# Kernel optimization log

Hardware: AMD Instinct MI355X
Metric: run time of the kernel (lower is better)

The kernel has to match this reference:

```python
import jax, jax.numpy as jnp
import numpy as np

B, D, H, C, P, HP = 65536, 256, 512, 10, 10, 128


def setup_inputs() -> dict:
    key = jax.random.key(0)
    ks = jax.random.split(key, 6)
    return {
        "x": jax.random.normal(ks[0], (B, D), jnp.float32),
        "Wt1": jax.random.normal(ks[1], (D, H), jnp.float32) * (1.0 / np.sqrt(D)),
        "bt1": jnp.zeros((H,), jnp.float32),
        "Wt2": jax.random.normal(ks[2], (H, C), jnp.float32) * (1.0 / np.sqrt(H)),
        "bt2": jnp.zeros((C,), jnp.float32),
        "Wp1": jax.random.normal(ks[3], (P, D, HP), jnp.float32) * (1.0 / np.sqrt(D)),
        "bp1": jnp.zeros((P, HP), jnp.float32),
        "Wp2": jax.random.normal(ks[4], (P, HP, C), jnp.float32) * (1.0 / np.sqrt(HP)),
        "bp2": jnp.zeros((P, C), jnp.float32),
        "repair_direction_dict": jax.random.randint(ks[5], (P, 2), 0, C, jnp.int32),
    }


def _get_bitmap(out, rdd):
    # torch.topk(out, 2): indices of the two largest logits per row
    _, idx = jax.lax.top_k(out, 2)                                  # [B, 2]
    # is_in[b, p] = all(idx[b] == rdd[p])  (exact top-2 pair match)
    is_in = jnp.all(idx[:, None, :] == rdd[None, :, :], axis=-1)     # [B, P]
    no_match = ~jnp.any(is_in, axis=-1)                              # [B]
    # fallback for unmatched rows: top-1 index equals rdd[:, 0]
    fallback = idx[:, :1] == rdd[None, :, 0]                         # [B, P]
    return jnp.where(no_match[:, None], fallback, is_in)             # bool [B, P]


def reference(x, Wt1, bt1, Wt2, bt2, Wp1, bp1, Wp2, bp2, repair_direction_dict):
    # target net forward: out = target_net(x)
    out = jnp.maximum(x @ Wt1 + bt1, 0.0) @ Wt2 + bt2                # [B, C]
    # bitmap computed under no_grad in the original -> stop_gradient
    bitmap = jax.lax.stop_gradient(
        _get_bitmap(out, repair_direction_dict)
    ).astype(out.dtype)                                              # [B, P]
    # each patch net runs on the FULL batch (as in the original), then the
    # bitmap gates the scatter-add combine: out[bits] += p_out[bits]
    h = jnp.maximum(jnp.einsum('bd,pdh->pbh', x, Wp1) + bp1[:, None, :], 0.0)  # [P, B, HP]
    p_out = jnp.einsum('pbh,phc->pbc', h, Wp2) + bp2[:, None, :]     # [P, B, C]
    return out + jnp.einsum('bp,pbc->bc', bitmap, p_out)             # [B, C]
```

## Files before the change

kernel.cpp:

```cpp
#include <hip/hip_runtime.h>

typedef unsigned int u32;
typedef unsigned short u16;
typedef _Float16 f16;
typedef __attribute__((ext_vector_type(8))) _Float16 f16x8;
typedef __attribute__((ext_vector_type(4))) float f32x4;

#define MARGIN 1e-2f
#define LSC 2048.0f
#define LSCI (1.0f/2048.0f)

__device__ __forceinline__ u16 f16b(float f) {
    return __builtin_bit_cast(u16, (f16)f);
}
__device__ __forceinline__ f32x4 MF(f16x8 a, f16x8 b, f32x4 c) {
    return __builtin_amdgcn_mfma_f32_16x16x32_f16(a, b, c, 0, 0, 0);
}
__device__ __forceinline__ uint4 pack8(const u16 v[8]) {
    uint4 pk;
    pk.x = (u32)v[0] | ((u32)v[1] << 16);
    pk.y = (u32)v[2] | ((u32)v[3] << 16);
    pk.z = (u32)v[4] | ((u32)v[5] << 16);
    pk.w = (u32)v[6] | ((u32)v[7] << 16);
    return pk;
}

__global__ __launch_bounds__(256) void conv_kernel(
    const float* __restrict__ Wt1, const float* __restrict__ Wp1,
    const float* __restrict__ Wt2, const float* __restrict__ Wp2,
    u16* __restrict__ wt1f, u16* __restrict__ wt1g, u16* __restrict__ wp1f,
    u16* __restrict__ wt2f, u16* __restrict__ wt2g, u16* __restrict__ wp2f,
    u32* __restrict__ gcnt)
{
    __shared__ float tile[64][68];
    const int t = threadIdx.x;
    const int b = blockIdx.x;

    if (b == 112) {
        if (t == 0) gcnt[0] = 0;
        for (int cc = t; cc < 1024; cc += 256) {
            int kk = cc >> 6, l = cc & 63, ln = l & 15, quad = l >> 4;
            u16 vh[8], vl[8];
            #pragma unroll
            for (int j = 0; j < 8; ++j) {
                int k = kk * 32 + quad * 8 + j;
                float f = (ln < 10) ? Wt2[k * 10 + ln] : 0.f;
                f16 h = (f16)f;
                vh[j] = __builtin_bit_cast(u16, h);
                vl[j] = f16b(LSC * (f - (float)h));
            }
            *(uint4*)(wt2f + kk * 512 + l * 8) = pack8(vh);
            *(uint4*)(wt2g + kk * 512 + l * 8) = pack8(vl);
        }
        for (int cc = t; cc < 2560; cc += 256) {
            int p = cc >> 8, rem = cc & 255, kk = rem >> 6, l = rem & 63;
            int ln = l & 15, quad = (l >> 4) & 3;
            u16 v[8];
            #pragma unroll
            for (int j = 0; j < 8; ++j) {
                int k = kk * 32 + quad * 8 + j;
                v[j] = f16b(ln < 10 ? Wp2[p * 1280 + k * 10 + ln] : 0.f);
            }
            *(uint4*)(wp2f + p * 2048 + kk * 512 + l * 8) = pack8(v);
        }
        return;
    }

    const float* src; int src_ld;
    u16 *dsth, *dstl; int nf0, kk0;
    if (b < 32) {
        int kt = b & 3, nt = b >> 2;
        src = Wt1 + (size_t)(kt * 64) * 512 + nt * 64; src_ld = 512;
        dsth = wt1f; dstl = wt1g; nf0 = nt * 4; kk0 = kt * 2;
    } else {
        int j = b - 32, p = j >> 3, r = j & 7;
        int kt = r & 3, nt = r >> 2;
        src = Wp1 + (size_t)p * 32768 + (size_t)(kt * 64) * 128 + nt * 64; src_ld = 128;
        dsth = wp1f + p * 32768; dstl = nullptr; nf0 = nt * 4; kk0 = kt * 2;
    }
    {
        const int kr = t >> 2, c0 = (t & 3) * 16;
        #pragma unroll
        for (int u = 0; u < 4; ++u) {
            float4 v = *(const float4*)(src + (size_t)kr * src_ld + c0 + u * 4);
            tile[kr][c0 + u*4 + 0] = v.x;
            tile[kr][c0 + u*4 + 1] = v.y;
            tile[kr][c0 + u*4 + 2] = v.z;
            tile[kr][c0 + u*4 + 3] = v.w;
        }
    }
    __syncthreads();
    #pragma unroll
    for (int s = 0; s < 2; ++s) {
        int cc = t + 256 * s;
        int l = cc & 63, fp = cc >> 6, nfl = fp >> 1, kkl = fp & 1;
        int ln = l & 15, quad = (l >> 4) & 3;
        int nloc = nfl * 16 + ln, kloc = kkl * 32 + quad * 8;
        u16 vh[8], vl[8];
        #pragma unroll
        for (int j = 0; j < 8; ++j) {
            float f = tile[kloc + j][nloc];
            f16 h = (f16)f;
            vh[j] = __builtin_bit_cast(u16, h);
            vl[j] = f16b(LSC * (f - (float)h));
        }
        size_t off = (size_t)((nf0 + nfl) * 8 + (kk0 + kkl)) * 512 + l * 8;
        *(uint4*)(dsth + off) = pack8(vh);
        if (dstl) *(uint4*)(dstl + off) = pack8(vl);
    }
}

__global__ __launch_bounds__(512, 4) void netsum_kernel(
    const float* __restrict__ x, const float* __restrict__ bt1,
    const float* __restrict__ bt2,
    const float* __restrict__ bp1, const float* __restrict__ bp2,
    const int* __restrict__ rdd,
    const u16* __restrict__ wt1f, const u16* __restrict__ wp1f,
    const u16* __restrict__ wt2f, const u16* __restrict__ wp2f,
    float* __restrict__ out, u32* __restrict__ gcnt, u32* __restrict__ glist)
{
    __shared__ u16 xf[64][264];
    __shared__ u16 hbuf[17408];
    __shared__ float lg[64][10];
    __shared__ float oacc[64][10];
    __shared__ u32 plist[10][64];
    __shared__ u32 pcnt[10];
    __shared__ int rdds[20];
    __shared__ u32 wq[40];
    __shared__ u32 nwork;

    const int t = threadIdx.x;
    const int lane = t & 63;
    const int w = t >> 6;
    const int ln = lane & 15;
    const int quad = lane >> 4;
    const int row0 = blockIdx.x * 64;

    if (t < 10) pcnt[t] = 0;
    if (t < 20) rdds[t] = rdd[t];
    if (t == 0) nwork = 0;
    for (int i = t; i < 640; i += 512) ((float*)oacc)[i] = 0.f;

    #pragma unroll
    for (int i = 0; i < 8; ++i) {
        int f = t + 512 * i;
        int r = f >> 6, c4 = f & 63;
        float4 v = *(const float4*)(x + (size_t)(row0 + r) * 256 + c4 * 4);
        u16 q0 = f16b(v.x), q1 = f16b(v.y), q2 = f16b(v.z), q3 = f16b(v.w);
        uint2 pw = { (u32)q0 | ((u32)q1 << 16), (u32)q2 | ((u32)q3 << 16) };
        *(uint2*)&xf[r][c4 * 4] = pw;
    }
    __syncthreads();

    f32x4 acc2 = (f32x4){0.f, 0.f, 0.f, 0.f};
    for (int hl = 0; hl < 2; ++hl) {
        f32x4 acc[4][2];
        #pragma unroll
        for (int m = 0; m < 4; ++m) {
            acc[m][0] = (f32x4){0.f,0.f,0.f,0.f};
            acc[m][1] = (f32x4){0.f,0.f,0.f,0.f};
        }
        const u16* bb = wt1f + (size_t)(hl * 16 + w * 2) * 4096 + lane * 8;
        for (int kk = 0; kk < 8; ++kk) {
            f16x8 b0 = *(const f16x8*)(bb + kk * 512);
            f16x8 b1 = *(const f16x8*)(bb + 4096 + kk * 512);
            #pragma unroll
            for (int m = 0; m < 4; ++m) {
                f16x8 a = *(const f16x8*)(&xf[m * 16 + ln][kk * 32 + quad * 8]);
                acc[m][0] = MF(a, b0, acc[m][0]);
                acc[m][1] = MF(a, b1, acc[m][1]);
            }
        }
        #pragma unroll
        for (int m = 0; m < 4; ++m)
            #pragma unroll
            for (int i2 = 0; i2 < 2; ++i2) {
                int nloc = w * 32 + i2 * 16 + ln;
                float bias = bt1[hl * 256 + nloc];
                #pragma unroll
                for (int r = 0; r < 4; ++r) {
                    float hv = acc[m][i2][r] + bias; hv = hv > 0.f ? hv : 0.f;
                    hbuf[(m * 16 + quad * 4 + r) * 264 + nloc] = f16b(hv);
                }
            }
        __syncthreads();
        if (w < 4) {
            #pragma unroll
            for (int kk = 0; kk < 8; ++kk) {
                f16x8 ha = *(const f16x8*)(&hbuf[(w * 16 + ln) * 264 + kk * 32 + quad * 8]);
                f16x8 wb = *(const f16x8*)(wt2f + (hl * 8 + kk) * 512 + lane * 8);
                acc2 = MF(ha, wb, acc2);
            }
        }
        __syncthreads();
    }
    if (w < 4 && ln < 10) {
        #pragma unroll
        for (int r = 0; r < 4; ++r)
            lg[w * 16 + quad * 4 + r][ln] = acc2[r] + bt2[ln];
    }
    __syncthreads();

    if (t < 64) {
        float l[10];
        #pragma unroll
        for (int c = 0; c < 10; ++c) l[c] = lg[t][c];
        float b0 = -1e30f; int i0 = 0;
        #pragma unroll
        for (int c = 0; c < 10; ++c) if (l[c] > b0) { b0 = l[c]; i0 = c; }
        float b1 = -1e30f; int i1 = 0;
        #pragma unroll
        for (int c = 0; c < 10; ++c) { if (c == i0) continue; if (l[c] > b1) { b1 = l[c]; i1 = c; } }
        float b2v = -1e30f;
        #pragma unroll
        for (int c = 0; c < 10; ++c) { if (c == i0 || c == i1) continue; if (l[c] > b2v) b2v = l[c]; }
        if (b0 - b1 < MARGIN || b1 - b2v < MARGIN) {
            u32 idx = atomicAdd(gcnt, 1u);
            glist[idx] = (u32)(row0 + t);
        }
        u32 exact = 0, fb = 0;
        #pragma unroll
        for (int p = 0; p < 10; ++p) {
            int a = rdds[2 * p], bq = rdds[2 * p + 1];
            if (i0 == a && i1 == bq) exact |= 1u << p;
            if (i0 == a)             fb    |= 1u << p;
        }
        u32 bits = exact ? exact : fb;
        while (bits) {
            int p = __ffs(bits) - 1;
            bits &= bits - 1;
            u32 idx = atomicAdd(&pcnt[p], 1u);
            plist[p][idx] = (u32)t;
        }
    }
    __syncthreads();
    if (t < 10) {
        int L = (int)pcnt[t];
        for (int base = 0; base < L; base += 16) {
            u32 e = atomicAdd(&nwork, 1u);
            wq[e] = ((u32)t << 8) | (u32)base;
        }
    }
    __syncthreads();

    {
        const u32 nw = nwork;
        for (u32 ii = w; ii < nw; ii += 8) {
            const u32 item = wq[ii];
            const int p = (int)(item >> 8), mbase = (int)(item & 255);
            const int Lp = (int)pcnt[p];
            const int mi = mbase + ln;
            const int arow = (mi < Lp) ? (int)plist[p][mi] : (int)plist[p][0];
            const u16* xr = &xf[arow][0];
            const u16* wb = wp1f + (size_t)p * 32768 + lane * 8;
            f32x4 pacc[8];
            #pragma unroll
            for (int i2 = 0; i2 < 8; ++i2) pacc[i2] = (f32x4){0.f,0.f,0.f,0.f};
            for (int kk = 0; kk < 8; ++kk) {
                f16x8 a = *(const f16x8*)(xr + kk * 32 + quad * 8);
                #pragma unroll
                for (int i2 = 0; i2 < 8; ++i2) {
                    f16x8 bb2 = *(const f16x8*)(wb + (i2 * 8 + kk) * 512);
                    pacc[i2] = MF(a, bb2, pacc[i2]);
                }
            }
            u16* hp = &hbuf[w * 2176];
            #pragma unroll
            for (int i2 = 0; i2 < 8; ++i2) {
                float bias = bp1[p * 128 + i2 * 16 + ln];
                #pragma unroll
                for (int r = 0; r < 4; ++r) {
                    float hv = pacc[i2][r] + bias; hv = hv > 0.f ? hv : 0.f;
                    hp[(quad * 4 + r) * 136 + i2 * 16 + ln] = f16b(hv);
                }
            }
            f32x4 po = (f32x4){0.f,0.f,0.f,0.f};
            #pragma unroll
            for (int kk = 0; kk < 4; ++kk) {
                f16x8 ha = *(const f16x8*)(&hp[ln * 136 + kk * 32 + quad * 8]);
                f16x8 wb2 = *(const f16x8*)(wp2f + p * 2048 + kk * 512 + lane * 8);
                po = MF(ha, wb2, po);
            }
            if (ln < 10) {
                float b2 = bp2[p * 10 + ln];
                #pragma unroll
                for (int r = 0; r < 4; ++r) {
                    int mi2 = mbase + quad * 4 + r;
                    if (mi2 < Lp)
                        atomicAdd(&oacc[plist[p][mi2]][ln], po[r] + b2);
                }
            }
        }
    }
    __syncthreads();

    for (int i = t; i < 640; i += 512)
        out[(size_t)row0 * 10 + i] = ((float*)lg)[i] + ((float*)oacc)[i];
}

__global__ __launch_bounds__(512, 1) void fix_kernel(
    const float* __restrict__ x, const float* __restrict__ bt1,
    const float* __restrict__ bt2,
    const float* __restrict__ bp1, const float* __restrict__ bp2,
    const int* __restrict__ rdd,
    const u16* __restrict__ wt1f, const u16* __restrict__ wt1g,
    const u16* __restrict__ wt2f, const u16* __restrict__ wt2g,
    const u16* __restrict__ wp1f, const u16* __restrict__ wp2f,
    const u32* __restrict__ gcnt, const u32* __restrict__ glist,
    float* __restrict__ out)
{
    __shared__ u16 xfh[64][264];
    __shared__ u16 xfl[64][264];
    __shared__ u16 hb2[2][16896];
    __shared__ float lg[64][10];
    __shared__ float oacc[64][10];
    __shared__ u32 rows[64];
    __shared__ u32 plist[10][64];
    __shared__ u32 pcnt[10];
    __shared__ int rdds[20];
    __shared__ u32 wq[40];
    __shared__ u32 nwork;

    const int t = threadIdx.x;
    const int lane = t & 63;
    const int w = t >> 6;
    const int ln = lane & 15;
    const int quad = lane >> 4;
    const u32 cnt = gcnt[0];
    if (t < 20) rdds[t] = rdd[t];

    for (u32 base = blockIdx.x * 64; base < cnt; base += gridDim.x * 64) {
        __syncthreads();
        const int R = (int)min(64u, cnt - base);
        if (t < 64) rows[t] = glist[base + (t < R ? t : 0)];
        if (t < 10) pcnt[t] = 0;
        if (t == 0) nwork = 0;
        for (int i = t; i < 640; i += 512) ((float*)oacc)[i] = 0.f;
        __syncthreads();

        #pragma unroll
        for (int i = 0; i < 8; ++i) {
            int f = t + 512 * i;
            int r = f >> 6, c4 = f & 63;
            float4 v = *(const float4*)(x + (size_t)rows[r] * 256 + c4 * 4);
            f16 h0 = (f16)v.x, h1 = (f16)v.y, h2 = (f16)v.z, h3 = (f16)v.w;
            u16 q0 = __builtin_bit_cast(u16, h0), q1 = __builtin_bit_cast(u16, h1);
            u16 q2 = __builtin_bit_cast(u16, h2), q3 = __builtin_bit_cast(u16, h3);
            u16 l0 = f16b(LSC * (v.x - (float)h0)), l1 = f16b(LSC * (v.y - (float)h1));
            u16 l2 = f16b(LSC * (v.z - (float)h2)), l3 = f16b(LSC * (v.w - (float)h3));
            uint2 hw = { (u32)q0 | ((u32)q1 << 16), (u32)q2 | ((u32)q3 << 16) };
            uint2 lw = { (u32)l0 | ((u32)l1 << 16), (u32)l2 | ((u32)l3 << 16) };
            *(uint2*)&xfh[r][c4 * 4] = hw;
            *(uint2*)&xfl[r][c4 * 4] = lw;
        }
        __syncthreads();

        f32x4 acc2h = (f32x4){0.f,0.f,0.f,0.f};
        f32x4 acc2s = (f32x4){0.f,0.f,0.f,0.f};
        for (int hl = 0; hl < 2; ++hl) {
            f32x4 accH[4][2], accS[4][2];
            #pragma unroll
            for (int m = 0; m < 4; ++m)
                #pragma unroll
                for (int i2 = 0; i2 < 2; ++i2) {
                    accH[m][i2] = (f32x4){0.f,0.f,0.f,0.f};
                    accS[m][i2] = (f32x4){0.f,0.f,0.f,0.f};
                }
            const size_t boff = (size_t)(hl * 16 + w * 2) * 4096 + lane * 8;
            const u16* bbh = wt1f + boff;
            const u16* bbl = wt1g + boff;
            for (int kk = 0; kk < 8; ++kk) {
                f16x8 bh0 = *(const f16x8*)(bbh + kk * 512);
                f16x8 bh1 = *(const f16x8*)(bbh + 4096 + kk * 512);
                f16x8 bl0 = *(const f16x8*)(bbl + kk * 512);
                f16x8 bl1 = *(const f16x8*)(bbl + 4096 + kk * 512);
                #pragma unroll
                for (int m = 0; m < 4; ++m) {
                    f16x8 ah = *(const f16x8*)(&xfh[m * 16 + ln][kk * 32 + quad * 8]);
                    f16x8 al = *(const f16x8*)(&xfl[m * 16 + ln][kk * 32 + quad * 8]);
                    accH[m][0] = MF(ah, bh0, accH[m][0]);
                    accS[m][0] = MF(ah, bl0, accS[m][0]);
                    accS[m][0] = MF(al, bh0, accS[m][0]);
                    accH[m][1] = MF(ah, bh1, accH[m][1]);
                    accS[m][1] = MF(ah, bl1, accS[m][1]);
                    accS[m][1] = MF(al, bh1, accS[m][1]);
                }
            }
            #pragma unroll
            for (int m = 0; m < 4; ++m)
                #pragma unroll
                for (int i2 = 0; i2 < 2; ++i2) {
                    int nloc = w * 32 + i2 * 16 + ln;
                    float bias = bt1[hl * 256 + nloc];
                    #pragma unroll
                    for (int r = 0; r < 4; ++r) {
                        float hv = accH[m][i2][r] + accS[m][i2][r] * LSCI + bias;
                        hv = hv > 0.f ? hv : 0.f;
                        f16 hh = (f16)hv;
                        int idx = (m * 16 + quad * 4 + r) * 264 + nloc;
                        hb2[0][idx] = __builtin_bit_cast(u16, hh);
                        hb2[1][idx] = f16b(LSC * (hv - (float)hh));
                    }
                }
            __syncthreads();
            if (w < 4) {
                #pragma unroll
                for (int kk = 0; kk < 8; ++kk) {
                    int hidx = (w * 16 + ln) * 264 + kk * 32 + quad * 8;
                    f16x8 hah = *(const f16x8*)(&hb2[0][hidx]);
                    f16x8 hal = *(const f16x8*)(&hb2[1][hidx]);
                    f16x8 wbh = *(const f16x8*)(wt2f + (hl * 8 + kk) * 512 + lane * 8);
                    f16x8 wbl = *(const f16x8*)(wt2g + (hl * 8 + kk) * 512 + lane * 8);
                    acc2h = MF(hah, wbh, acc2h);
                    acc2s = MF(hah, wbl, acc2s);
                    acc2s = MF(hal, wbh, acc2s);
                }
            }
            __syncthreads();
        }
        if (w < 4 && ln < 10) {
            #pragma unroll
            for (int r = 0; r < 4; ++r)
                lg[w * 16 + quad * 4 + r][ln] = acc2h[r] + acc2s[r] * LSCI + bt2[ln];
        }
        __syncthreads();

        if (t < R) {
            float l[10];
            #pragma unroll
            for (int c = 0; c < 10; ++c) l[c] = lg[t][c];
            float b0 = -1e30f; int i0 = 0;
            #pragma unroll
            for (int c = 0; c < 10; ++c) if (l[c] > b0) { b0 = l[c]; i0 = c; }
            float b1 = -1e30f; int i1 = 0;
            #pragma unroll
            for (int c = 0; c < 10; ++c) { if (c == i0) continue; if (l[c] > b1) { b1 = l[c]; i1 = c; } }
            u32 exact = 0, fb = 0;
            #pragma unroll
            for (int p = 0; p < 10; ++p) {
                int a = rdds[2 * p], bq = rdds[2 * p + 1];
                if (i0 == a && i1 == bq) exact |= 1u << p;
                if (i0 == a)             fb    |= 1u << p;
            }
            u32 bits = exact ? exact : fb;
            while (bits) {
                int p = __ffs(bits) - 1;
                bits &= bits - 1;
                u32 idx = atomicAdd(&pcnt[p], 1u);
                plist[p][idx] = (u32)t;
            }
        }
        __syncthreads();
        if (t < 10) {
            int L = (int)pcnt[t];
            for (int b2 = 0; b2 < L; b2 += 16) {
                u32 e = atomicAdd(&nwork, 1u);
                wq[e] = ((u32)t << 8) | (u32)b2;
            }
        }
        __syncthreads();

        {
            const u32 nw = nwork;
            u16* hbuf = &hb2[0][0];
            for (u32 ii = w; ii < nw; ii += 8) {
                const u32 item = wq[ii];
                const int p = (int)(item >> 8), mbase = (int)(item & 255);
                const int Lp = (int)pcnt[p];
                const int mi = mbase + ln;
                const int arow = (mi < Lp) ? (int)plist[p][mi] : (int)plist[p][0];
                const u16* xr = &xfh[arow][0];
                const u16* wb = wp1f + (size_t)p * 32768 + lane * 8;
                f32x4 pacc[8];
                #pragma unroll
                for (int i2 = 0; i2 < 8; ++i2) pacc[i2] = (f32x4){0.f,0.f,0.f,0.f};
                for (int kk = 0; kk < 8; ++kk) {
                    f16x8 a = *(const f16x8*)(xr + kk * 32 + quad * 8);
                    #pragma unroll
                    for (int i2 = 0; i2 < 8; ++i2) {
                        f16x8 bb2 = *(const f16x8*)(wb + (i2 * 8 + kk) * 512);
                        pacc[i2] = MF(a, bb2, pacc[i2]);
                    }
                }
                u16* hp = &hbuf[w * 2176];
                #pragma unroll
                for (int i2 = 0; i2 < 8; ++i2) {
                    float bias = bp1[p * 128 + i2 * 16 + ln];
                    #pragma unroll
                    for (int r = 0; r < 4; ++r) {
                        float hv = pacc[i2][r] + bias; hv = hv > 0.f ? hv : 0.f;
                        hp[(quad * 4 + r) * 136 + i2 * 16 + ln] = f16b(hv);
                    }
                }
                f32x4 po = (f32x4){0.f,0.f,0.f,0.f};
                #pragma unroll
                for (int kk = 0; kk < 4; ++kk) {
                    f16x8 ha = *(const f16x8*)(&hp[ln * 136 + kk * 32 + quad * 8]);
                    f16x8 wb2 = *(const f16x8*)(wp2f + p * 2048 + kk * 512 + lane * 8);
                    po = MF(ha, wb2, po);
                }
                if (ln < 10) {
                    float b2 = bp2[p * 10 + ln];
                    #pragma unroll
                    for (int r = 0; r < 4; ++r) {
                        int mi2 = mbase + quad * 4 + r;
                        if (mi2 < Lp)
                            atomicAdd(&oacc[plist[p][mi2]][ln], po[r] + b2);
                    }
                }
            }
        }
        __syncthreads();

        for (int i = t; i < R * 10; i += 512) {
            int r = i / 10, c = i % 10;
            out[(size_t)rows[r] * 10 + c] = lg[r][c] + oacc[r][c];
        }
    }
}

extern "C" void kernel_launch(void* const* d_in, const int* in_sizes, int n_in,
                              void* d_out, int out_size, void* d_ws, size_t ws_size,
                              hipStream_t stream) {
    const float* x   = (const float*)d_in[0];
    const float* Wt1 = (const float*)d_in[1];
    const float* bt1 = (const float*)d_in[2];
    const float* Wt2 = (const float*)d_in[3];
    const float* bt2 = (const float*)d_in[4];
    const float* Wp1 = (const float*)d_in[5];
    const float* bp1 = (const float*)d_in[6];
    const float* Wp2 = (const float*)d_in[7];
    const float* bp2 = (const float*)d_in[8];
    const int* rdd = (const int*)d_in[9];
    float* out = (float*)d_out;

    u16* wt1f = (u16*)d_ws;
    u16* wt1g = wt1f + 131072;
    u16* wp1f = wt1g + 131072;
    u16* wt2f = wp1f + 327680;
    u16* wt2g = wt2f + 8192;
    u16* wp2f = wt2g + 8192;
    u32* gcnt  = (u32*)(wp2f + 20480);
    u32* glist = gcnt + 16;

    hipLaunchKernelGGL(conv_kernel, dim3(113), dim3(256), 0, stream,
                       Wt1, Wp1, Wt2, Wp2, wt1f, wt1g, wp1f, wt2f, wt2g, wp2f, gcnt);
    hipLaunchKernelGGL(netsum_kernel, dim3(1024), dim3(512), 0, stream,
                       x, bt1, bt2, bp1, bp2, rdd,
                       wt1f, wp1f, wt2f, wp2f, out, gcnt, glist);
    hipLaunchKernelGGL(fix_kernel, dim3(128), dim3(512), 0, stream,
                       x, bt1, bt2, bp1, bp2, rdd,
                       wt1f, wt1g, wt2f, wt2g, wp1f, wp2f,
                       gcnt, glist, out);
}
```

Measured before the change: 215.3 us.

## Cut accumulator register pressure and software-pipeline weight loads in MLP kernels

The target first layer now runs in four 128-wide hidden chunks with one accumulator column per wave instead of two 256-wide chunks, and the weight fragment for the next k step is prefetched into a register. The patch layer-1 GEMM is split into two groups of four accumulators, each with double-buffered weight loads, so fewer registers are live and global load latency is hidden. The goal is to raise occupancy under the launch bounds and overlap loads with MFMA work. The fix kernel grid is doubled and its k loop is unrolled. The trade-off is twice as many barrier/layer-2 rounds in the target path.

```diff
diff --git a/kernel.cpp b/kernel.cpp
--- a/kernel.cpp
+++ b/kernel.cpp
@@ -120,7 +120,7 @@
     float* __restrict__ out, u32* __restrict__ gcnt, u32* __restrict__ glist)
 {
     __shared__ u16 xf[64][264];
-    __shared__ u16 hbuf[17408];
+    __shared__ u16 scratch[17408];
     __shared__ float lg[64][10];
     __shared__ float oacc[64][10];
     __shared__ u32 plist[10][64];
@@ -153,42 +153,41 @@
     __syncthreads();
 
     f32x4 acc2 = (f32x4){0.f, 0.f, 0.f, 0.f};
-    for (int hl = 0; hl < 2; ++hl) {
-        f32x4 acc[4][2];
-        #pragma unroll
-        for (int m = 0; m < 4; ++m) {
-            acc[m][0] = (f32x4){0.f,0.f,0.f,0.f};
-            acc[m][1] = (f32x4){0.f,0.f,0.f,0.f};
-        }
-        const u16* bb = wt1f + (size_t)(hl * 16 + w * 2) * 4096 + lane * 8;
+    u16* hq = scratch;
+    for (int q = 0; q < 4; ++q) {
+        f32x4 acc[4];
+        #pragma unroll
+        for (int m = 0; m < 4; ++m) acc[m] = (f32x4){0.f,0.f,0.f,0.f};
+        const u16* bb = wt1f + (size_t)((q * 8 + w) * 8) * 512 + (size_t)lane * 8;
+        f16x8 wc = *(const f16x8*)bb;
+        #pragma unroll
         for (int kk = 0; kk < 8; ++kk) {
-            f16x8 b0 = *(const f16x8*)(bb + kk * 512);
-            f16x8 b1 = *(const f16x8*)(bb + 4096 + kk * 512);
+            f16x8 wn = wc;
+            if (kk < 7) wn = *(const f16x8*)(bb + (kk + 1) * 512);
             #pragma unroll
             for (int m = 0; m < 4; ++m) {
                 f16x8 a = *(const f16x8*)(&xf[m * 16 + ln][kk * 32 + quad * 8]);
-                acc[m][0] = MF(a, b0, acc[m][0]);
-                acc[m][1] = MF(a, b1, acc[m][1]);
-            }
-        }
-        #pragma unroll
-        for (int m = 0; m < 4; ++m)
-            #pragma unroll
-            for (int i2 = 0; i2 < 2; ++i2) {
-                int nloc = w * 32 + i2 * 16 + ln;
-                float bias = bt1[hl * 256 + nloc];
+                acc[m] = MF(a, wc, acc[m]);
+            }
+            wc = wn;
+        }
+        {
+            const int nloc = w * 16 + ln;
+            const float bias = bt1[q * 128 + nloc];
+            #pragma unroll
+            for (int m = 0; m < 4; ++m)
                 #pragma unroll
                 for (int r = 0; r < 4; ++r) {
-                    float hv = acc[m][i2][r] + bias; hv = hv > 0.f ? hv : 0.f;
-                    hbuf[(m * 16 + quad * 4 + r) * 264 + nloc] = f16b(hv);
-                }
-            }
+                    float hv = acc[m][r] + bias; hv = hv > 0.f ? hv : 0.f;
+                    hq[(m * 16 + quad * 4 + r) * 136 + nloc] = f16b(hv);
+                }
+        }
         __syncthreads();
         if (w < 4) {
             #pragma unroll
-            for (int kk = 0; kk < 8; ++kk) {
-                f16x8 ha = *(const f16x8*)(&hbuf[(w * 16 + ln) * 264 + kk * 32 + quad * 8]);
-                f16x8 wb = *(const f16x8*)(wt2f + (hl * 8 + kk) * 512 + lane * 8);
+            for (int kk2 = 0; kk2 < 4; ++kk2) {
+                f16x8 ha = *(const f16x8*)(&hq[(w * 16 + ln) * 136 + kk2 * 32 + quad * 8]);
+                f16x8 wb = *(const f16x8*)(wt2f + (q * 4 + kk2) * 512 + lane * 8);
                 acc2 = MF(ha, wb, acc2);
             }
         }
@@ -252,26 +251,41 @@
             const int mi = mbase + ln;
             const int arow = (mi < Lp) ? (int)plist[p][mi] : (int)plist[p][0];
             const u16* xr = &xf[arow][0];
-            const u16* wb = wp1f + (size_t)p * 32768 + lane * 8;
-            f32x4 pacc[8];
-            #pragma unroll
-            for (int i2 = 0; i2 < 8; ++i2) pacc[i2] = (f32x4){0.f,0.f,0.f,0.f};
-            for (int kk = 0; kk < 8; ++kk) {
-                f16x8 a = *(const f16x8*)(xr + kk * 32 + quad * 8);
-                #pragma unroll
-                for (int i2 = 0; i2 < 8; ++i2) {
-                    f16x8 bb2 = *(const f16x8*)(wb + (i2 * 8 + kk) * 512);
-                    pacc[i2] = MF(a, bb2, pacc[i2]);
-                }
-            }
-            u16* hp = &hbuf[w * 2176];
-            #pragma unroll
-            for (int i2 = 0; i2 < 8; ++i2) {
-                float bias = bp1[p * 128 + i2 * 16 + ln];
-                #pragma unroll
-                for (int r = 0; r < 4; ++r) {
-                    float hv = pacc[i2][r] + bias; hv = hv > 0.f ? hv : 0.f;
-                    hp[(quad * 4 + r) * 136 + i2 * 16 + ln] = f16b(hv);
+            const u16* wb = wp1f + (size_t)p * 32768 + (size_t)lane * 8;
+            u16* hp = &scratch[w * 2176];
+            #pragma unroll
+            for (int g = 0; g < 2; ++g) {
+                f32x4 acc4[4];
+                #pragma unroll
+                for (int i2 = 0; i2 < 4; ++i2) acc4[i2] = (f32x4){0.f,0.f,0.f,0.f};
+                f16x8 wc4[4];
+                #pragma unroll
+                for (int i2 = 0; i2 < 4; ++i2)
+                    wc4[i2] = *(const f16x8*)(wb + ((g * 4 + i2) * 8 + 0) * 512);
+                #pragma unroll
+                for (int kk = 0; kk < 8; ++kk) {
+                    f16x8 wn4[4];
+                    #pragma unroll
+                    for (int i2 = 0; i2 < 4; ++i2) {
+                        wn4[i2] = wc4[i2];
+                        if (kk < 7)
+                            wn4[i2] = *(const f16x8*)(wb + ((g * 4 + i2) * 8 + kk + 1) * 512);
+                    }
+                    f16x8 a = *(const f16x8*)(xr + kk * 32 + quad * 8);
+                    #pragma unroll
+                    for (int i2 = 0; i2 < 4; ++i2) acc4[i2] = MF(a, wc4[i2], acc4[i2]);
+                    #pragma unroll
+                    for (int i2 = 0; i2 < 4; ++i2) wc4[i2] = wn4[i2];
+                }
+                #pragma unroll
+                for (int i2 = 0; i2 < 4; ++i2) {
+                    const int i2g = g * 4 + i2;
+                    float bias = bp1[p * 128 + i2g * 16 + ln];
+                    #pragma unroll
+                    for (int r = 0; r < 4; ++r) {
+                        float hv = acc4[i2][r] + bias; hv = hv > 0.f ? hv : 0.f;
+                        hp[(quad * 4 + r) * 136 + i2g * 16 + ln] = f16b(hv);
+                    }
                 }
             }
             f32x4 po = (f32x4){0.f,0.f,0.f,0.f};
@@ -366,9 +380,10 @@
                     accH[m][i2] = (f32x4){0.f,0.f,0.f,0.f};
                     accS[m][i2] = (f32x4){0.f,0.f,0.f,0.f};
                 }
-            const size_t boff = (size_t)(hl * 16 + w * 2) * 4096 + lane * 8;
+            const size_t boff = (size_t)(hl * 16 + w * 2) * 4096 + (size_t)lane * 8;
             const u16* bbh = wt1f + boff;
             const u16* bbl = wt1g + boff;
+            #pragma unroll
             for (int kk = 0; kk < 8; ++kk) {
                 f16x8 bh0 = *(const f16x8*)(bbh + kk * 512);
                 f16x8 bh1 = *(const f16x8*)(bbh + 4096 + kk * 512);
@@ -470,26 +485,41 @@
                 const int mi = mbase + ln;
                 const int arow = (mi < Lp) ? (int)plist[p][mi] : (int)plist[p][0];
                 const u16* xr = &xfh[arow][0];
-                const u16* wb = wp1f + (size_t)p * 32768 + lane * 8;
-                f32x4 pacc[8];
-                #pragma unroll
-                for (int i2 = 0; i2 < 8; ++i2) pacc[i2] = (f32x4){0.f,0.f,0.f,0.f};
-                for (int kk = 0; kk < 8; ++kk) {
-                    f16x8 a = *(const f16x8*)(xr + kk * 32 + quad * 8);
-                    #pragma unroll
-                    for (int i2 = 0; i2 < 8; ++i2) {
-                        f16x8 bb2 = *(const f16x8*)(wb + (i2 * 8 + kk) * 512);
-                        pacc[i2] = MF(a, bb2, pacc[i2]);
+                const u16* wb = wp1f + (size_t)p * 32768 + (size_t)lane * 8;
+                u16* hp = &hbuf[w * 2176];
+                #pragma unroll
+                for (int g = 0; g < 2; ++g) {
+                    f32x4 acc4[4];
+                    #pragma unroll
+                    for (int i2 = 0; i2 < 4; ++i2) acc4[i2] = (f32x4){0.f,0.f,0.f,0.f};
+                    f16x8 wc4[4];
+                    #pragma unroll
+                    for (int i2 = 0; i2 < 4; ++i2)
+                        wc4[i2] = *(const f16x8*)(wb + ((g * 4 + i2) * 8 + 0) * 512);
+                    #pragma unroll
+                    for (int kk = 0; kk < 8; ++kk) {
+                        f16x8 wn4[4];
+                        #pragma unroll
+                        for (int i2 = 0; i2 < 4; ++i2) {
+                            wn4[i2] = wc4[i2];
+                            if (kk < 7)
+                                wn4[i2] = *(const f16x8*)(wb + ((g * 4 + i2) * 8 + kk + 1) * 512);
+                        }
+                        f16x8 a = *(const f16x8*)(xr + kk * 32 + quad * 8);
+                        #pragma unroll
+                        for (int i2 = 0; i2 < 4; ++i2) acc4[i2] = MF(a, wc4[i2], acc4[i2]);
+                        #pragma unroll
+                        for (int i2 = 0; i2 < 4; ++i2) wc4[i2] = wn4[i2];
                     }
-                }
-                u16* hp = &hbuf[w * 2176];
-                #pragma unroll
-                for (int i2 = 0; i2 < 8; ++i2) {
-                    float bias = bp1[p * 128 + i2 * 16 + ln];
-                    #pragma unroll
-                    for (int r = 0; r < 4; ++r) {
-                        float hv = pacc[i2][r] + bias; hv = hv > 0.f ? hv : 0.f;
-                        hp[(quad * 4 + r) * 136 + i2 * 16 + ln] = f16b(hv);
+                    #pragma unroll
+                    for (int i2 = 0; i2 < 4; ++i2) {
+                        const int i2g = g * 4 + i2;
+                        float bias = bp1[p * 128 + i2g * 16 + ln];
+                        #pragma unroll
+                        for (int r = 0; r < 4; ++r) {
+                            float hv = acc4[i2][r] + bias; hv = hv > 0.f ? hv : 0.f;
+                            hp[(quad * 4 + r) * 136 + i2g * 16 + ln] = f16b(hv);
+                        }
                     }
                 }
                 f32x4 po = (f32x4){0.f,0.f,0.f,0.f};
@@ -548,7 +578,7 @@
     hipLaunchKernelGGL(netsum_kernel, dim3(1024), dim3(512), 0, stream,
                        x, bt1, bt2, bp1, bp2, rdd,
                        wt1f, wp1f, wt2f, wp2f, out, gcnt, glist);
-    hipLaunchKernelGGL(fix_kernel, dim3(128), dim3(512), 0, stream,
+    hipLaunchKernelGGL(fix_kernel, dim3(256), dim3(512), 0, stream,
                        x, bt1, bt2, bp1, bp2, rdd,
                        wt1f, wt1g, wt2f, wt2g, wp1f, wp2f,
                        gcnt, glist, out);
```

Result: faster. 198.5 us (-7.8%).

## Software-pipeline weight loads across MFMA loops and restructure target layer into quarters

Applied to the files above, without the earlier changes.

The target-net first layer now runs in four 128-column quarters: each wave owns 16 columns, and the weight fragments for the next quarter are prefetched into registers while the current quarter's MFMAs run. Patch-net and fix-kernel inner loops get double-buffered register loads of weight fragments, with the second-layer weights hoisted ahead of the loop. The LDS scratch padding changes from 264/136 to 140 strides, and the fix kernel grid doubles. This is meant to hide global-load latency behind MFMA work, at the cost of higher register pressure and more barriers per block.

```diff
diff --git a/kernel.cpp b/kernel.cpp
--- a/kernel.cpp
+++ b/kernel.cpp
@@ -110,6 +110,56 @@
     }
 }
 
+#define PLD(S, KK) \
+    S##0 = *(const f16x8*)(wb + (0*8+(KK))*512); \
+    S##1 = *(const f16x8*)(wb + (1*8+(KK))*512); \
+    S##2 = *(const f16x8*)(wb + (2*8+(KK))*512); \
+    S##3 = *(const f16x8*)(wb + (3*8+(KK))*512); \
+    S##4 = *(const f16x8*)(wb + (4*8+(KK))*512); \
+    S##5 = *(const f16x8*)(wb + (5*8+(KK))*512); \
+    S##6 = *(const f16x8*)(wb + (6*8+(KK))*512); \
+    S##7 = *(const f16x8*)(wb + (7*8+(KK))*512);
+#define PMF(S, KK) { f16x8 Ax_ = *(const f16x8*)(xr + (KK)*32 + quad*8); \
+    a0=MF(Ax_,S##0,a0); a1=MF(Ax_,S##1,a1); a2=MF(Ax_,S##2,a2); a3=MF(Ax_,S##3,a3); \
+    a4=MF(Ax_,S##4,a4); a5=MF(Ax_,S##5,a5); a6=MF(Ax_,S##6,a6); a7=MF(Ax_,S##7,a7); }
+#define HPS(AC, I) { float bias_ = bp1[p*128 + (I)*16 + ln]; \
+    _Pragma("unroll") for (int r_=0;r_<4;++r_){ float hv_=(AC)[r_]+bias_; hv_=hv_>0.f?hv_:0.f; \
+        hp[(quad*4+r_)*140 + (I)*16+ln]=f16b(hv_);} }
+#define LH(KK2) (*(const f16x8*)(&hp[ln*140 + (KK2)*32 + quad*8]))
+
+#define LDB(Q,KK) (*(const f16x8*)(wt1f + (size_t)((((Q)*8 + w)*8 + (KK)))*512 + lane*8))
+#define LDT(Q,K2) (*(const f16x8*)(wt2f + (size_t)((Q)*4+(K2))*512 + lane*8))
+#define L1MF(BB, KK) { \
+    f16x8 A0_=*(const f16x8*)(&xf[0*16+ln][(KK)*32+quad*8]); \
+    f16x8 A1_=*(const f16x8*)(&xf[1*16+ln][(KK)*32+quad*8]); \
+    f16x8 A2_=*(const f16x8*)(&xf[2*16+ln][(KK)*32+quad*8]); \
+    f16x8 A3_=*(const f16x8*)(&xf[3*16+ln][(KK)*32+quad*8]); \
+    ac0=MF(A0_,BB,ac0); ac1=MF(A1_,BB,ac1); ac2=MF(A2_,BB,ac2); ac3=MF(A3_,BB,ac3); }
+#define HQS(AC, M) { _Pragma("unroll") for (int r_=0;r_<4;++r_){ \
+    float hv_=(AC)[r_]+bias; hv_=hv_>0.f?hv_:0.f; \
+    hq[((M)*16+quad*4+r_)*140 + nloc]=f16b(hv_);} }
+#define QUARTER(Q, NL) { \
+    f32x4 ac0={0.f,0.f,0.f,0.f}, ac1=ac0, ac2=ac0, ac3=ac0; \
+    L1MF(b0,0); if (NL) b0 = LDB((Q)+1,0); \
+    L1MF(b1,1); if (NL) b1 = LDB((Q)+1,1); \
+    L1MF(b2,2); if (NL) b2 = LDB((Q)+1,2); \
+    L1MF(b3,3); if (NL) b3 = LDB((Q)+1,3); \
+    L1MF(b4,4); if (NL) b4 = LDB((Q)+1,4); \
+    L1MF(b5,5); if (NL) b5 = LDB((Q)+1,5); \
+    L1MF(b6,6); if (NL) b6 = LDB((Q)+1,6); \
+    L1MF(b7,7); if (NL) b7 = LDB((Q)+1,7); \
+    { const int nloc = w*16+ln; const float bias = bt1[(Q)*128+nloc]; \
+      HQS(ac0,0); HQS(ac1,1); HQS(ac2,2); HQS(ac3,3); } \
+    __syncthreads(); \
+    if (w < 4) { \
+        acc2 = MF(*(const f16x8*)(&hq[(w*16+ln)*140 + 0*32 + quad*8]), t0, acc2); \
+        acc2 = MF(*(const f16x8*)(&hq[(w*16+ln)*140 + 1*32 + quad*8]), t1, acc2); \
+        acc2 = MF(*(const f16x8*)(&hq[(w*16+ln)*140 + 2*32 + quad*8]), t2, acc2); \
+        acc2 = MF(*(const f16x8*)(&hq[(w*16+ln)*140 + 3*32 + quad*8]), t3, acc2); \
+        if (NL) { t0 = LDT((Q)+1,0); t1 = LDT((Q)+1,1); t2 = LDT((Q)+1,2); t3 = LDT((Q)+1,3); } \
+    } \
+    __syncthreads(); }
+
 __global__ __launch_bounds__(512, 4) void netsum_kernel(
     const float* __restrict__ x, const float* __restrict__ bt1,
     const float* __restrict__ bt2,
@@ -120,7 +170,7 @@
     float* __restrict__ out, u32* __restrict__ gcnt, u32* __restrict__ glist)
 {
     __shared__ u16 xf[64][264];
-    __shared__ u16 hbuf[17408];
+    __shared__ u16 scratch[17920];
     __shared__ float lg[64][10];
     __shared__ float oacc[64][10];
     __shared__ u32 plist[10][64];
@@ -150,50 +200,18 @@
         uint2 pw = { (u32)q0 | ((u32)q1 << 16), (u32)q2 | ((u32)q3 << 16) };
         *(uint2*)&xf[r][c4 * 4] = pw;
     }
+    f16x8 b0 = LDB(0,0), b1 = LDB(0,1), b2 = LDB(0,2), b3 = LDB(0,3);
+    f16x8 b4 = LDB(0,4), b5 = LDB(0,5), b6 = LDB(0,6), b7 = LDB(0,7);
+    f16x8 t0 = {}, t1 = {}, t2 = {}, t3 = {};
+    if (w < 4) { t0 = LDT(0,0); t1 = LDT(0,1); t2 = LDT(0,2); t3 = LDT(0,3); }
     __syncthreads();
 
     f32x4 acc2 = (f32x4){0.f, 0.f, 0.f, 0.f};
-    for (int hl = 0; hl < 2; ++hl) {
-        f32x4 acc[4][2];
-        #pragma unroll
-        for (int m = 0; m < 4; ++m) {
-            acc[m][0] = (f32x4){0.f,0.f,0.f,0.f};
-            acc[m][1] = (f32x4){0.f,0.f,0.f,0.f};
-        }
-        const u16* bb = wt1f + (size_t)(hl * 16 + w * 2) * 4096 + lane * 8;
-        for (int kk = 0; kk < 8; ++kk) {
-            f16x8 b0 = *(const f16x8*)(bb + kk * 512);
-            f16x8 b1 = *(const f16x8*)(bb + 4096 + kk * 512);
-            #pragma unroll
-            for (int m = 0; m < 4; ++m) {
-                f16x8 a = *(const f16x8*)(&xf[m * 16 + ln][kk * 32 + quad * 8]);
-                acc[m][0] = MF(a, b0, acc[m][0]);
-                acc[m][1] = MF(a, b1, acc[m][1]);
-            }
-        }
-        #pragma unroll
-        for (int m = 0; m < 4; ++m)
-            #pragma unroll
-            for (int i2 = 0; i2 < 2; ++i2) {
-                int nloc = w * 32 + i2 * 16 + ln;
-                float bias = bt1[hl * 256 + nloc];
-                #pragma unroll
-                for (int r = 0; r < 4; ++r) {
-                    float hv = acc[m][i2][r] + bias; hv = hv > 0.f ? hv : 0.f;
-                    hbuf[(m * 16 + quad * 4 + r) * 264 + nloc] = f16b(hv);
-                }
-            }
-        __syncthreads();
-        if (w < 4) {
-            #pragma unroll
-            for (int kk = 0; kk < 8; ++kk) {
-                f16x8 ha = *(const f16x8*)(&hbuf[(w * 16 + ln) * 264 + kk * 32 + quad * 8]);
-                f16x8 wb = *(const f16x8*)(wt2f + (hl * 8 + kk) * 512 + lane * 8);
-                acc2 = MF(ha, wb, acc2);
-            }
-        }
-        __syncthreads();
-    }
+    u16* hq = scratch;
+    QUARTER(0, 1)
+    QUARTER(1, 1)
+    QUARTER(2, 1)
+    QUARTER(3, 0)
     if (w < 4 && ln < 10) {
         #pragma unroll
         for (int r = 0; r < 4; ++r)
@@ -205,16 +223,16 @@
         float l[10];
         #pragma unroll
         for (int c = 0; c < 10; ++c) l[c] = lg[t][c];
-        float b0 = -1e30f; int i0 = 0;
-        #pragma unroll
-        for (int c = 0; c < 10; ++c) if (l[c] > b0) { b0 = l[c]; i0 = c; }
-        float b1 = -1e30f; int i1 = 0;
-        #pragma unroll
-        for (int c = 0; c < 10; ++c) { if (c == i0) continue; if (l[c] > b1) { b1 = l[c]; i1 = c; } }
+        float b0v = -1e30f; int i0 = 0;
+        #pragma unroll
+        for (int c = 0; c < 10; ++c) if (l[c] > b0v) { b0v = l[c]; i0 = c; }
+        float b1v = -1e30f; int i1 = 0;
+        #pragma unroll
+        for (int c = 0; c < 10; ++c) { if (c == i0) continue; if (l[c] > b1v) { b1v = l[c]; i1 = c; } }
         float b2v = -1e30f;
         #pragma unroll
         for (int c = 0; c < 10; ++c) { if (c == i0 || c == i1) continue; if (l[c] > b2v) b2v = l[c]; }
-        if (b0 - b1 < MARGIN || b1 - b2v < MARGIN) {
+        if (b0v - b1v < MARGIN || b1v - b2v < MARGIN) {
             u32 idx = atomicAdd(gcnt, 1u);
             glist[idx] = (u32)(row0 + t);
         }
@@ -252,35 +270,30 @@
             const int mi = mbase + ln;
             const int arow = (mi < Lp) ? (int)plist[p][mi] : (int)plist[p][0];
             const u16* xr = &xf[arow][0];
-            const u16* wb = wp1f + (size_t)p * 32768 + lane * 8;
-            f32x4 pacc[8];
-            #pragma unroll
-            for (int i2 = 0; i2 < 8; ++i2) pacc[i2] = (f32x4){0.f,0.f,0.f,0.f};
-            for (int kk = 0; kk < 8; ++kk) {
-                f16x8 a = *(const f16x8*)(xr + kk * 32 + quad * 8);
-                #pragma unroll
-                for (int i2 = 0; i2 < 8; ++i2) {
-                    f16x8 bb2 = *(const f16x8*)(wb + (i2 * 8 + kk) * 512);
-                    pacc[i2] = MF(a, bb2, pacc[i2]);
-                }
-            }
-            u16* hp = &hbuf[w * 2176];
-            #pragma unroll
-            for (int i2 = 0; i2 < 8; ++i2) {
-                float bias = bp1[p * 128 + i2 * 16 + ln];
-                #pragma unroll
-                for (int r = 0; r < 4; ++r) {
-                    float hv = pacc[i2][r] + bias; hv = hv > 0.f ? hv : 0.f;
-                    hp[(quad * 4 + r) * 136 + i2 * 16 + ln] = f16b(hv);
-                }
-            }
+            const u16* wb = wp1f + (size_t)p * 32768 + (size_t)lane * 8;
+            f16x8 w20 = *(const f16x8*)(wp2f + p * 2048 + 0 * 512 + lane * 8);
+            f16x8 w21 = *(const f16x8*)(wp2f + p * 2048 + 1 * 512 + lane * 8);
+            f16x8 w22 = *(const f16x8*)(wp2f + p * 2048 + 2 * 512 + lane * 8);
+            f16x8 w23 = *(const f16x8*)(wp2f + p * 2048 + 3 * 512 + lane * 8);
+            f32x4 a0={0.f,0.f,0.f,0.f}, a1=a0, a2=a0, a3=a0, a4=a0, a5=a0, a6=a0, a7=a0;
+            f16x8 c0,c1,c2,c3,c4,c5,c6,c7, d0,d1,d2,d3,d4,d5,d6,d7;
+            PLD(c,0);
+            PLD(d,1); PMF(c,0);
+            PLD(c,2); PMF(d,1);
+            PLD(d,3); PMF(c,2);
+            PLD(c,4); PMF(d,3);
+            PLD(d,5); PMF(c,4);
+            PLD(c,6); PMF(d,5);
+            PLD(d,7); PMF(c,6);
+            PMF(d,7);
+            u16* hp = scratch + w * 2240;
+            HPS(a0,0); HPS(a1,1); HPS(a2,2); HPS(a3,3);
+            HPS(a4,4); HPS(a5,5); HPS(a6,6); HPS(a7,7);
             f32x4 po = (f32x4){0.f,0.f,0.f,0.f};
-            #pragma unroll
-            for (int kk = 0; kk < 4; ++kk) {
-                f16x8 ha = *(const f16x8*)(&hp[ln * 136 + kk * 32 + quad * 8]);
-                f16x8 wb2 = *(const f16x8*)(wp2f + p * 2048 + kk * 512 + lane * 8);
-                po = MF(ha, wb2, po);
-            }
+            po = MF(LH(0), w20, po);
+            po = MF(LH(1), w21, po);
+            po = MF(LH(2), w22, po);
+            po = MF(LH(3), w23, po);
             if (ln < 10) {
                 float b2 = bp2[p * 10 + ln];
                 #pragma unroll
@@ -297,6 +310,23 @@
     for (int i = t; i < 640; i += 512)
         out[(size_t)row0 * 10 + i] = ((float*)lg)[i] + ((float*)oacc)[i];
 }
+
+#define FLD(S,KK) \
+    S##h0 = *(const f16x8*)(bbh + (KK)*512); \
+    S##h1 = *(const f16x8*)(bbh + 4096 + (KK)*512); \
+    S##l0 = *(const f16x8*)(bbl + (KK)*512); \
+    S##l1 = *(const f16x8*)(bbl + 4096 + (KK)*512);
+#define FCP(S,KK) { _Pragma("unroll") for (int m_=0;m_<4;++m_){ \
+    f16x8 ah_=*(const f16x8*)(&xfh[m_*16+ln][(KK)*32+quad*8]); \
+    f16x8 al_=*(const f16x8*)(&xfl[m_*16+ln][(KK)*32+quad*8]); \
+    accH[m_][0]=MF(ah_,S##h0,accH[m_][0]); accS[m_][0]=MF(ah_,S##l0,accS[m_][0]); accS[m_][0]=MF(al_,S##h0,accS[m_][0]); \
+    accH[m_][1]=MF(ah_,S##h1,accH[m_][1]); accS[m_][1]=MF(ah_,S##l1,accS[m_][1]); accS[m_][1]=MF(al_,S##h1,accS[m_][1]); } }
+#define F2L(WH, WL, KK) \
+    WH = *(const f16x8*)(wt2f + (hl*8+(KK))*512 + lane*8); \
+    WL = *(const f16x8*)(wt2g + (hl*8+(KK))*512 + lane*8);
+#define F2C(WH, WL, KK) { int hidx_=(w*16+ln)*264 + (KK)*32 + quad*8; \
+    f16x8 hah_=*(const f16x8*)(&hb2[0][hidx_]); f16x8 hal_=*(const f16x8*)(&hb2[1][hidx_]); \
+    acc2h=MF(hah_,WH,acc2h); acc2s=MF(hah_,WL,acc2s); acc2s=MF(hal_,WH,acc2s); }
 
 __global__ __launch_bounds__(512, 1) void fix_kernel(
     const float* __restrict__ x, const float* __restrict__ bt1,
@@ -366,26 +396,19 @@
                     accH[m][i2] = (f32x4){0.f,0.f,0.f,0.f};
                     accS[m][i2] = (f32x4){0.f,0.f,0.f,0.f};
                 }
-            const size_t boff = (size_t)(hl * 16 + w * 2) * 4096 + lane * 8;
+            const size_t boff = (size_t)(hl * 16 + w * 2) * 4096 + (size_t)lane * 8;
             const u16* bbh = wt1f + boff;
             const u16* bbl = wt1g + boff;
-            for (int kk = 0; kk < 8; ++kk) {
-                f16x8 bh0 = *(const f16x8*)(bbh + kk * 512);
-                f16x8 bh1 = *(const f16x8*)(bbh + 4096 + kk * 512);
-                f16x8 bl0 = *(const f16x8*)(bbl + kk * 512);
-                f16x8 bl1 = *(const f16x8*)(bbl + 4096 + kk * 512);
-                #pragma unroll
-                for (int m = 0; m < 4; ++m) {
-                    f16x8 ah = *(const f16x8*)(&xfh[m * 16 + ln][kk * 32 + quad * 8]);
-                    f16x8 al = *(const f16x8*)(&xfl[m * 16 + ln][kk * 32 + quad * 8]);
-                    accH[m][0] = MF(ah, bh0, accH[m][0]);
-                    accS[m][0] = MF(ah, bl0, accS[m][0]);
-                    accS[m][0] = MF(al, bh0, accS[m][0]);
-                    accH[m][1] = MF(ah, bh1, accH[m][1]);
-                    accS[m][1] = MF(ah, bl1, accS[m][1]);
-                    accS[m][1] = MF(al, bh1, accS[m][1]);
-                }
-            }
+            f16x8 ch0, ch1, cl0, cl1, nh0, nh1, nl0, nl1;
+            FLD(c,0);
+            FLD(n,1); FCP(c,0);
+            FLD(c,2); FCP(n,1);
+            FLD(n,3); FCP(c,2);
+            FLD(c,4); FCP(n,3);
+            FLD(n,5); FCP(c,4);
+            FLD(c,6); FCP(n,5);
+            FLD(n,7); FCP(c,6);
+            FCP(n,7);
             #pragma unroll
             for (int m = 0; m < 4; ++m)
                 #pragma unroll
@@ -404,17 +427,16 @@
                 }
             __syncthreads();
             if (w < 4) {
-                #pragma unroll
-                for (int kk = 0; kk < 8; ++kk) {
-                    int hidx = (w * 16 + ln) * 264 + kk * 32 + quad * 8;
-                    f16x8 hah = *(const f16x8*)(&hb2[0][hidx]);
-                    f16x8 hal = *(const f16x8*)(&hb2[1][hidx]);
-                    f16x8 wbh = *(const f16x8*)(wt2f + (hl * 8 + kk) * 512 + lane * 8);
-                    f16x8 wbl = *(const f16x8*)(wt2g + (hl * 8 + kk) * 512 + lane * 8);
-                    acc2h = MF(hah, wbh, acc2h);
-                    acc2s = MF(hah, wbl, acc2s);
-                    acc2s = MF(hal, wbh, acc2s);
-                }
+                f16x8 whc, wlc, whn, wln;
+                F2L(whc, wlc, 0);
+                F2L(whn, wln, 1); F2C(whc, wlc, 0);
+                F2L(whc, wlc, 2); F2C(whn, wln, 1);
+                F2L(whn, wln, 3); F2C(whc, wlc, 2);
+                F2L(whc, wlc, 4); F2C(whn, wln, 3);
+                F2L(whn, wln, 5); F2C(whc, wlc, 4);
+                F2L(whc, wlc, 6); F2C(whn, wln, 5);
+                F2L(whn, wln, 7); F2C(whc, wlc, 6);
+                F2C(whn, wln, 7);
             }
             __syncthreads();
         }
@@ -429,12 +451,12 @@
             float l[10];
             #pragma unroll
             for (int c = 0; c < 10; ++c) l[c] = lg[t][c];
-            float b0 = -1e30f; int i0 = 0;
-            #pragma unroll
-            for (int c = 0; c < 10; ++c) if (l[c] > b0) { b0 = l[c]; i0 = c; }
-            float b1 = -1e30f; int i1 = 0;
-            #pragma unroll
-            for (int c = 0; c < 10; ++c) { if (c == i0) continue; if (l[c] > b1) { b1 = l[c]; i1 = c; } }
+            float b0v = -1e30f; int i0 = 0;
+            #pragma unroll
+            for (int c = 0; c < 10; ++c) if (l[c] > b0v) { b0v = l[c]; i0 = c; }
+            float b1v = -1e30f; int i1 = 0;
+            #pragma unroll
+            for (int c = 0; c < 10; ++c) { if (c == i0) continue; if (l[c] > b1v) { b1v = l[c]; i1 = c; } }
             u32 exact = 0, fb = 0;
             #pragma unroll
             for (int p = 0; p < 10; ++p) {
@@ -453,16 +475,16 @@
         __syncthreads();
         if (t < 10) {
             int L = (int)pcnt[t];
-            for (int b2 = 0; b2 < L; b2 += 16) {
+            for (int b2i = 0; b2i < L; b2i += 16) {
                 u32 e = atomicAdd(&nwork, 1u);
-                wq[e] = ((u32)t << 8) | (u32)b2;
+                wq[e] = ((u32)t << 8) | (u32)b2i;
             }
         }
         __syncthreads();
 
         {
             const u32 nw = nwork;
-            u16* hbuf = &hb2[0][0];
+            u16* hbase = &hb2[0][0];
             for (u32 ii = w; ii < nw; ii += 8) {
                 const u32 item = wq[ii];
                 const int p = (int)(item >> 8), mbase = (int)(item & 255);
@@ -470,35 +492,30 @@
                 const int mi = mbase + ln;
                 const int arow = (mi < Lp) ? (int)plist[p][mi] : (int)plist[p][0];
                 const u16* xr = &xfh[arow][0];
-                const u16* wb = wp1f + (size_t)p * 32768 + lane * 8;
-                f32x4 pacc[8];
-                #pragma unroll
-                for (int i2 = 0; i2 < 8; ++i2) pacc[i2] = (f32x4){0.f,0.f,0.f,0.f};
-                for (int kk = 0; kk < 8; ++kk) {
-                    f16x8 a = *(const f16x8*)(xr + kk * 32 + quad * 8);
-                    #pragma unroll
-                    for (int i2 = 0; i2 < 8; ++i2) {
-                        f16x8 bb2 = *(const f16x8*)(wb + (i2 * 8 + kk) * 512);
-                        pacc[i2] = MF(a, bb2, pacc[i2]);
-                    }
-                }
-                u16* hp = &hbuf[w * 2176];
-                #pragma unroll
-                for (int i2 = 0; i2 < 8; ++i2) {
-                    float bias = bp1[p * 128 + i2 * 16 + ln];
-                    #pragma unroll
-                    for (int r = 0; r < 4; ++r) {
-                        float hv = pacc[i2][r] + bias; hv = hv > 0.f ? hv : 0.f;
-                        hp[(quad * 4 + r) * 136 + i2 * 16 + ln] = f16b(hv);
-                    }
-                }
+                const u16* wb = wp1f + (size_t)p * 32768 + (size_t)lane * 8;
+                f16x8 w20 = *(const f16x8*)(wp2f + p * 2048 + 0 * 512 + lane * 8);
+                f16x8 w21 = *(const f16x8*)(wp2f + p * 2048 + 1 * 512 + lane * 8);
+                f16x8 w22 = *(const f16x8*)(wp2f + p * 2048 + 2 * 512 + lane * 8);
+                f16x8 w23 = *(const f16x8*)(wp2f + p * 2048 + 3 * 512 + lane * 8);
+                f32x4 a0={0.f,0.f,0.f,0.f}, a1=a0, a2=a0, a3=a0, a4=a0, a5=a0, a6=a0, a7=a0;
+                f16x8 c0,c1,c2,c3,c4,c5,c6,c7, d0,d1,d2,d3,d4,d5,d6,d7;
+                PLD(c,0);
+                PLD(d,1); PMF(c,0);
+                PLD(c,2); PMF(d,1);
+                PLD(d,3); PMF(c,2);
+                PLD(c,4); PMF(d,3);
+                PLD(d,5); PMF(c,4);
+                PLD(c,6); PMF(d,5);
+                PLD(d,7); PMF(c,6);
+                PMF(d,7);
+                u16* hp = hbase + w * 2240;
+                HPS(a0,0); HPS(a1,1); HPS(a2,2); HPS(a3,3);
+                HPS(a4,4); HPS(a5,5); HPS(a6,6); HPS(a7,7);
                 f32x4 po = (f32x4){0.f,0.f,0.f,0.f};
-                #pragma unroll
-                for (int kk = 0; kk < 4; ++kk) {
-                    f16x8 ha = *(const f16x8*)(&hp[ln * 136 + kk * 32 + quad * 8]);
-                    f16x8 wb2 = *(const f16x8*)(wp2f + p * 2048 + kk * 512 + lane * 8);
-                    po = MF(ha, wb2, po);
-                }
+                po = MF(LH(0), w20, po);
+                po = MF(LH(1), w21, po);
+                po = MF(LH(2), w22, po);
+                po = MF(LH(3), w23, po);
                 if (ln < 10) {
                     float b2 = bp2[p * 10 + ln];
                     #pragma unroll
@@ -548,7 +565,7 @@
     hipLaunchKernelGGL(netsum_kernel, dim3(1024), dim3(512), 0, stream,
                        x, bt1, bt2, bp1, bp2, rdd,
                        wt1f, wp1f, wt2f, wp2f, out, gcnt, glist);
-    hipLaunchKernelGGL(fix_kernel, dim3(128), dim3(512), 0, stream,
+    hipLaunchKernelGGL(fix_kernel, dim3(256), dim3(512), 0, stream,
                        x, bt1, bt2, bp1, bp2, rdd,
                        wt1f, wt1g, wt2f, wt2g, wp1f, wp2f,
                        gcnt, glist, out);
```

New measurement: 242.4 us. +12.6%, slower.
